# Kernel tuning notes

Measured on AMD Instinct MI355X. Metric: run time of the kernel, lower is better.

The kernel has to match this reference:

```python
import jax, jax.numpy as jnp
import numpy as np

N = 100000
E = 1600000
NODE_DIM = 64
H = 128
NUM_LAYERS = 3
NUM_CLASSES = 6
NUM_GRAPHS = 512
LN_EPS = 1e-5


def setup_inputs() -> dict:
    key = jax.random.key(0)
    ks = jax.random.split(key, 16)
    s = 0.05
    x = jax.random.normal(ks[0], (N, NODE_DIM), jnp.float32)
    edge_index = jax.random.randint(ks[1], (2, E), 0, N, dtype=jnp.int64)
    batch = jnp.sort(jax.random.randint(ks[2], (N,), 0, NUM_GRAPHS, dtype=jnp.int64))
    return {
        "x": x,
        "edge_index": edge_index,
        "batch": batch,
        "proj_w": jax.random.normal(ks[3], (NODE_DIM, H), jnp.float32) * s,
        "proj_b": jnp.zeros((H,), jnp.float32),
        "lin_l_w": jax.random.normal(ks[4], (NUM_LAYERS, H, H), jnp.float32) * s,
        "lin_l_b": jnp.zeros((NUM_LAYERS, H), jnp.float32),
        "lin_r_w": jax.random.normal(ks[5], (NUM_LAYERS, H, H), jnp.float32) * s,
        "ln_g": jnp.ones((NUM_LAYERS, H), jnp.float32),
        "ln_b": jnp.zeros((NUM_LAYERS, H), jnp.float32),
        "gate_w1": jax.random.normal(ks[6], (H, H // 2), jnp.float32) * s,
        "gate_b1": jnp.zeros((H // 2,), jnp.float32),
        "gate_w2": jax.random.normal(ks[7], (H // 2, 1), jnp.float32) * s,
        "gate_b2": jnp.zeros((1,), jnp.float32),
        "cls_w1": jax.random.normal(ks[8], (H, H // 2), jnp.float32) * s,
        "cls_b1": jnp.zeros((H // 2,), jnp.float32),
        "cls_w2": jax.random.normal(ks[9], (H // 2, NUM_CLASSES), jnp.float32) * s,
        "cls_b2": jnp.zeros((NUM_CLASSES,), jnp.float32),
    }


def _layer_norm(x, g, b):
    mu = jnp.mean(x, axis=-1, keepdims=True)
    var = jnp.mean(jnp.square(x - mu), axis=-1, keepdims=True)
    return (x - mu) * jax.lax.rsqrt(var + LN_EPS) * g + b


def _sage_mean_aggr(x, src, dst):
    # mean of source node features grouped by destination node
    summed = jax.ops.segment_sum(x[src], dst, num_segments=N)  # [N,H]
    deg = jax.ops.segment_sum(jnp.ones((E,), x.dtype), dst, num_segments=N)
    return summed / jnp.maximum(deg, 1.0)[:, None]


def reference(x, edge_index, batch, proj_w, proj_b, lin_l_w, lin_l_b, lin_r_w,
              ln_g, ln_b, gate_w1, gate_b1, gate_w2, gate_b2,
              cls_w1, cls_b1, cls_w2, cls_b2):
    src, dst = edge_index[0], edge_index[1]
    h = jax.nn.relu(x @ proj_w + proj_b)  # [N,H]
    for l in range(NUM_LAYERS):
        r = h
        aggr = _sage_mean_aggr(h, src, dst)
        # PyG SAGEConv: lin_l(aggregated) + lin_r(self), bias only in lin_l
        h = aggr @ lin_l_w[l] + lin_l_b[l] + h @ lin_r_w[l]
        h = _layer_norm(h, ln_g[l], ln_b[l])
        h = jax.nn.elu(h)
        h = h + r  # dropout is identity in eval mode
    # GlobalAttention pooling: segment softmax over nodes per graph
    gate = (jax.nn.relu(h @ gate_w1 + gate_b1) @ gate_w2 + gate_b2)[:, 0]  # [N]
    gmax = jax.ops.segment_max(gate, batch, num_segments=NUM_GRAPHS)
    eg = jnp.exp(gate - gmax[batch])
    denom = jax.ops.segment_sum(eg, batch, num_segments=NUM_GRAPHS)
    alpha = eg / denom[batch]  # [N]
    pooled = jax.ops.segment_sum(h * alpha[:, None], batch, num_segments=NUM_GRAPHS)  # [G,H]
    out = jax.nn.relu(pooled @ cls_w1 + cls_b1) @ cls_w2 + cls_b2  # [G,C]
    return out
```

## Files before the change

### kernel.cpp

```cpp
#include <hip/hip_runtime.h>
#include <hip/hip_fp16.h>
#include <math.h>

#define N_NODES   100000
#define N_EDGES   1600000
#define NDIM      64
#define H         128
#define NUM_LAYERS 3
#define NUM_CLASSES 6
#define NUM_GRAPHS 512
#define LN_EPS    1e-5f
#define NBKT      391
#define SCAP      5376
#define BPAD      136

typedef _Float16 f16x8 __attribute__((ext_vector_type(8)));
typedef float    f32x4 __attribute__((ext_vector_type(4)));

__device__ __forceinline__ int idx_at(const int* raw, int is64, int i) {
    return is64 ? raw[2 * (long long)i] : raw[i];
}
__device__ __forceinline__ int lower_bound(const int* a, int n, int v) {
    int lo = 0, hi = n;
    while (lo < hi) { int m = (lo + hi) >> 1; if (a[m] < v) lo = m + 1; else hi = m; }
    return lo;
}

__global__ void k_detect(const int* eraw, const int* braw, int* flags) {
    if (threadIdx.x == 0 && blockIdx.x == 0) {
        int e64 = 1;
        for (int i = 1; i < 128; i += 2) if (eraw[i] != 0) { e64 = 0; break; }
        flags[0] = e64;
        flags[1] = (braw[N_NODES - 1] == 0) ? 1 : 0;
    }
}

__global__ void k_init(int* bcnt) {
    int i = blockIdx.x * blockDim.x + threadIdx.x;
    if (i < 512) bcnt[i] = 0;
}

__global__ void k_conv_batch(const int* braw, const int* flags, int* batch32) {
    int i = blockIdx.x * blockDim.x + threadIdx.x;
    if (i < N_NODES) batch32[i] = idx_at(braw, flags[1], i);
}

__global__ __launch_bounds__(256) void k_bhist(const int* eraw, const int* flags, int* bcnt) {
    __shared__ int c[512];
    int tid = threadIdx.x;
    for (int i = tid; i < 512; i += 256) c[i] = 0;
    __syncthreads();
    int f = flags[0];
    int stride = gridDim.x * 256;
    for (int e = blockIdx.x * 256 + tid; e < N_EDGES; e += stride) {
        int d = idx_at(eraw, f, N_EDGES + e);
        atomicAdd(&c[d >> 8], 1);
    }
    __syncthreads();
    for (int i = tid; i < 512; i += 256) if (c[i]) atomicAdd(&bcnt[i], c[i]);
}

__global__ void k_bscan(const int* bcnt, int* boff, int* bcursor) {
    __shared__ int sh[512];
    int tid = threadIdx.x;
    int v = bcnt[tid];
    sh[tid] = v;
    __syncthreads();
    for (int off = 1; off < 512; off <<= 1) {
        int u = (tid >= off) ? sh[tid - off] : 0;
        __syncthreads();
        sh[tid] += u;
        __syncthreads();
    }
    int excl = sh[tid] - v;
    boff[tid] = excl;
    bcursor[tid] = excl;
    if (tid == 511) boff[512] = sh[511];
}

#define EPB 4096
__global__ __launch_bounds__(256) void k_bucket(const int* eraw, const int* flags,
                                                int* bcursor, unsigned int* br) {
    __shared__ int cnt[512];
    __shared__ int lcur[512];
    int tid = threadIdx.x;
    int f = flags[0];
    int base = blockIdx.x * EPB;
    int se[16], de[16];
#pragma unroll
    for (int j = 0; j < 16; ++j) {
        int e = base + j * 256 + tid;
        if (e < N_EDGES) {
            se[j] = idx_at(eraw, f, e);
            de[j] = idx_at(eraw, f, N_EDGES + e);
        } else de[j] = -1;
    }
    for (int i = tid; i < 512; i += 256) cnt[i] = 0;
    __syncthreads();
#pragma unroll
    for (int j = 0; j < 16; ++j)
        if (de[j] >= 0) atomicAdd(&cnt[de[j] >> 8], 1);
    __syncthreads();
    for (int i = tid; i < 512; i += 256)
        lcur[i] = cnt[i] ? atomicAdd(&bcursor[i], cnt[i]) : 0;
    __syncthreads();
#pragma unroll
    for (int j = 0; j < 16; ++j)
        if (de[j] >= 0) {
            int pos = atomicAdd(&lcur[de[j] >> 8], 1);
            br[pos] = ((unsigned int)(de[j] & 255) << 24) | (unsigned int)se[j];
        }
}

__global__ __launch_bounds__(256) void k_csr_tail(const unsigned int* br, const int* boff,
                                                  int* rowptr, int* col) {
    __shared__ int d256[256];
    __shared__ int sc[256];
    __shared__ int cbuf[SCAP];
    int b = blockIdx.x;
    int tid = threadIdx.x;
    int lo = boff[b], hi = boff[b + 1];
    int wsize = hi - lo;
    d256[tid] = 0;
    __syncthreads();
    for (int i = lo + tid; i < hi; i += 256)
        atomicAdd(&d256[br[i] >> 24], 1);
    __syncthreads();
    int v = d256[tid];
    sc[tid] = v;
    __syncthreads();
    for (int off = 1; off < 256; off <<= 1) {
        int u = (tid >= off) ? sc[tid - off] : 0;
        __syncthreads();
        sc[tid] += u;
        __syncthreads();
    }
    int excl = sc[tid] - v;
    int node = (b << 8) + tid;
    if (node < N_NODES) rowptr[node] = lo + excl;
    if (b == NBKT - 1 && tid == 0) rowptr[N_NODES] = N_EDGES;
    __syncthreads();
    d256[tid] = excl;
    __syncthreads();
    if (wsize <= SCAP) {
        for (int i = lo + tid; i < hi; i += 256) {
            unsigned int r = br[i];
            int p = atomicAdd(&d256[r >> 24], 1);
            cbuf[p] = (int)(r & 0xFFFFFF);
        }
        __syncthreads();
        for (int j = tid; j < wsize; j += 256) col[lo + j] = cbuf[j] << 8;
    } else {
        for (int i = lo + tid; i < hi; i += 256) {
            unsigned int r = br[i];
            int p = atomicAdd(&d256[r >> 24], 1);
            col[lo + p] = (int)(r & 0xFFFFFF) << 8;
        }
    }
}

__global__ void k_prepw(const float* __restrict__ lin_l_w, const float* __restrict__ lin_r_w,
                        const float* __restrict__ gate_w1,
                        __half* __restrict__ W16t, __half* __restrict__ W16g) {
    int i = blockIdx.x * 256 + threadIdx.x;
    if (i < NUM_LAYERS * 128 * 256) {
        int l = i >> 15;
        int rem = i & 32767;
        int n = rem >> 8;
        int k = rem & 255;
        float v = (k < 128) ? lin_l_w[(size_t)l * 16384 + k * 128 + n]
                            : lin_r_w[(size_t)l * 16384 + (k - 128) * 128 + n];
        W16t[(size_t)l * 32768 + n * 256 + k] = __float2half(v);
    } else if (i < NUM_LAYERS * 128 * 256 + 64 * 128) {
        int idx = i - NUM_LAYERS * 128 * 256;
        int n = idx >> 7;
        int k = idx & 127;
        W16g[n * 128 + k] = __float2half(gate_w1[k * 64 + n]);
    }
}

__global__ __launch_bounds__(256) void k_gemm_proj(const float* __restrict__ A,
                                                   const float* __restrict__ W,
                                                   const float* __restrict__ bias,
                                                   __half* __restrict__ C16,
                                                   int nrows, int K) {
    __shared__ float As_t[32][68];
    __shared__ float Ws[32 * 128];
    int tid = threadIdx.x;
    int row0 = blockIdx.x * 64;
    int tr = tid >> 4;
    int tc = tid & 15;
    int c0 = tc * 8;
    float acc[4][8];
#pragma unroll
    for (int i = 0; i < 4; ++i)
#pragma unroll
        for (int j = 0; j < 8; ++j) acc[i][j] = 0.f;

    for (int kc = 0; kc < K; kc += 32) {
        __syncthreads();
#pragma unroll
        for (int it = 0; it < 2; ++it) {
            int idx = tid + it * 256;
            int r = idx >> 3, c4 = idx & 7;
            int gr = row0 + r;
            float4 v = make_float4(0.f, 0.f, 0.f, 0.f);
            if (gr < nrows) v = *(const float4*)(A + (size_t)gr * K + kc + c4 * 4);
            As_t[c4 * 4 + 0][r] = v.x;
            As_t[c4 * 4 + 1][r] = v.y;
            As_t[c4 * 4 + 2][r] = v.z;
            As_t[c4 * 4 + 3][r] = v.w;
        }
#pragma unroll
        for (int it = 0; it < 4; ++it) {
            int idx = tid + it * 256;
            int r = idx >> 5, c4 = idx & 31;
            *(float4*)(&Ws[r * 128 + c4 * 4]) = *(const float4*)(W + (size_t)(kc + r) * 128 + c4 * 4);
        }
        __syncthreads();
#pragma unroll
        for (int k = 0; k < 32; ++k) {
            float4 a4 = *(const float4*)(&As_t[k][tr * 4]);
            float a[4] = {a4.x, a4.y, a4.z, a4.w};
            float4 w0 = *(const float4*)(&Ws[k * 128 + c0]);
            float4 w1 = *(const float4*)(&Ws[k * 128 + c0 + 4]);
            float w[8] = {w0.x, w0.y, w0.z, w0.w, w1.x, w1.y, w1.z, w1.w};
#pragma unroll
            for (int i = 0; i < 4; ++i)
#pragma unroll
                for (int j = 0; j < 8; ++j) acc[i][j] += a[i] * w[j];
        }
    }
    float bv[8];
#pragma unroll
    for (int j = 0; j < 8; ++j) bv[j] = bias[c0 + j];
#pragma unroll
    for (int i = 0; i < 4; ++i) {
        int gr = row0 + tr * 4 + i;
        if (gr < nrows) {
            float o[8];
#pragma unroll
            for (int j = 0; j < 8; ++j) o[j] = fmaxf(acc[i][j] + bv[j], 0.f);
            __half2 p[4];
#pragma unroll
            for (int j = 0; j < 8; j += 2) p[j / 2] = __floats2half2_rn(o[j], o[j + 1]);
            *(float4*)(C16 + (size_t)gr * 128 + c0) = *(float4*)p;
        }
    }
}

__global__ __launch_bounds__(256) void k_gate_mfma(const __half* __restrict__ h16,
                                                   const __half* __restrict__ W16g,
                                                   const float* __restrict__ b1,
                                                   const float* __restrict__ w2,
                                                   const float* __restrict__ b2,
                                                   float* __restrict__ gate) {
    __shared__ __half Bs[64 * BPAD];
    int tid = threadIdx.x;
    int wave = tid >> 6, lane = tid & 63;
    int s = lane & 15, quad = lane >> 4;
    int row0 = blockIdx.x * 64 + wave * 16;
    int arow = row0 + s;
    if (arow >= N_NODES) arow = N_NODES - 1;

#pragma unroll
    for (int it = 0; it < 4; ++it) {
        int idx = tid + it * 256;
        int n = idx >> 4, ch = idx & 15;
        *(float4*)(&Bs[n * BPAD + ch * 8]) = *(const float4*)(W16g + (size_t)n * 128 + ch * 8);
    }
    __syncthreads();

    f32x4 acc[4];
#pragma unroll
    for (int c = 0; c < 4; ++c) acc[c] = (f32x4){0.f, 0.f, 0.f, 0.f};

    const __half* aptr = h16 + (size_t)arow * H;
#pragma unroll
    for (int kc = 0; kc < 128; kc += 32) {
        f16x8 afrag = *(const f16x8*)(aptr + kc + quad * 8);
#pragma unroll
        for (int c = 0; c < 4; ++c) {
            f16x8 bfrag = *(const f16x8*)(&Bs[(c * 16 + s) * BPAD + kc + quad * 8]);
            acc[c] = __builtin_amdgcn_mfma_f32_16x16x32_f16(afrag, bfrag, acc[c], 0, 0, 0);
        }
    }
    float part[4] = {0.f, 0.f, 0.f, 0.f};
#pragma unroll
    for (int c = 0; c < 4; ++c) {
        float bv = b1[c * 16 + s];
        float wv = w2[c * 16 + s];
#pragma unroll
        for (int i = 0; i < 4; ++i)
            part[i] += fmaxf(acc[c][i] + bv, 0.f) * wv;
    }
#pragma unroll
    for (int off = 1; off < 16; off <<= 1) {
#pragma unroll
        for (int i = 0; i < 4; ++i) part[i] += __shfl_xor(part[i], off);
    }
    if (s == 0) {
        float b2v = b2[0];
#pragma unroll
        for (int i = 0; i < 4; ++i) {
            int r = row0 + quad * 4 + i;
            if (r < N_NODES) gate[r] = part[i] + b2v;
        }
    }
}

__global__ __launch_bounds__(64) void k_softmax_g(float* __restrict__ gate,
                                                  const int* __restrict__ batch32,
                                                  float* __restrict__ gsum) {
    int g = blockIdx.x;
    int lane = threadIdx.x;
    int n0 = lower_bound(batch32, N_NODES, g);
    int n1 = lower_bound(batch32, N_NODES, g + 1);
    float m = -INFINITY;
    for (int n = n0 + lane; n < n1; n += 64) m = fmaxf(m, gate[n]);
#pragma unroll
    for (int off = 32; off >= 1; off >>= 1) m = fmaxf(m, __shfl_xor(m, off));
    float s = 0.f;
    for (int n = n0 + lane; n < n1; n += 64) {
        float e = expf(gate[n] - m);
        gate[n] = e;
        s += e;
    }
#pragma unroll
    for (int off = 32; off >= 1; off >>= 1) s += __shfl_xor(s, off);
    if (lane == 0) gsum[g] = s;
}

__global__ __launch_bounds__(256) void k_pool_g(const __half* __restrict__ h16,
                                                const float* __restrict__ eg,
                                                const float* __restrict__ gsum,
                                                const int* __restrict__ batch32,
                                                float* __restrict__ pooled) {
    __shared__ float sacc[256];
    int g = blockIdx.x;
    int tid = threadIdx.x;
    int c = tid & 127;
    int p = tid >> 7;
    int n0 = lower_bound(batch32, N_NODES, g);
    int n1 = lower_bound(batch32, N_NODES, g + 1);
    float acc = 0.f;
    for (int n = n0 + p; n < n1; n += 2)
        acc += eg[n] * __half2float(h16[(size_t)n * H + c]);
    sacc[tid] = acc;
    __syncthreads();
    if (tid < 128) {
        float s = gsum[g];
        float v = sacc[tid] + sacc[tid + 128];
        pooled[(size_t)g * H + tid] = (n1 > n0) ? v / s : 0.f;
    }
}

__global__ __launch_bounds__(256) void k_layer_mfma(const __half* __restrict__ t16,
                                                    __half* __restrict__ h16,
                                                    const __half* __restrict__ W16t,
                                                    const float* __restrict__ bl,
                                                    const float* __restrict__ g,
                                                    const float* __restrict__ bb) {
    __shared__ __half Bs[128 * BPAD];
    int tid = threadIdx.x;
    int wave = tid >> 6, lane = tid & 63;
    int s = lane & 15, quad = lane >> 4;
    int row0 = blockIdx.x * 64;
    int wrow0 = row0 + wave * 16;
    int arow = wrow0 + s;
    if (arow >= N_NODES) arow = N_NODES - 1;

    f32x4 acc[8];
#pragma unroll
    for (int c = 0; c < 8; ++c) acc[c] = (f32x4){0.f, 0.f, 0.f, 0.f};

#pragma unroll
    for (int ph = 0; ph < 2; ++ph) {
        __syncthreads();
#pragma unroll
        for (int it = 0; it < 8; ++it) {
            int idx = tid + it * 256;
            int n = idx >> 4, ch = idx & 15;
            *(float4*)(&Bs[n * BPAD + ch * 8]) =
                *(const float4*)(W16t + (size_t)n * 256 + ph * 128 + ch * 8);
        }
        __syncthreads();
        const __half* aptr = (ph ? h16 : t16) + (size_t)arow * H;
#pragma unroll
        for (int kk = 0; kk < 128; kk += 32) {
            f16x8 afrag = *(const f16x8*)(aptr + kk + quad * 8);
#pragma unroll
            for (int c = 0; c < 8; ++c) {
                f16x8 bfrag = *(const f16x8*)(&Bs[(c * 16 + s) * BPAD + kk + quad * 8]);
                acc[c] = __builtin_amdgcn_mfma_f32_16x16x32_f16(afrag, bfrag, acc[c], 0, 0, 0);
            }
        }
    }

    float y[8][4];
    float sm[4] = {0.f, 0.f, 0.f, 0.f}, sq[4] = {0.f, 0.f, 0.f, 0.f};
#pragma unroll
    for (int c = 0; c < 8; ++c) {
        float bv = bl[c * 16 + s];
#pragma unroll
        for (int i = 0; i < 4; ++i) {
            float v = acc[c][i] + bv;
            y[c][i] = v;
            sm[i] += v;
            sq[i] += v * v;
        }
    }
#pragma unroll
    for (int off = 1; off < 16; off <<= 1) {
#pragma unroll
        for (int i = 0; i < 4; ++i) {
            sm[i] += __shfl_xor(sm[i], off);
            sq[i] += __shfl_xor(sq[i], off);
        }
    }
    float mean[4], rstd[4];
#pragma unroll
    for (int i = 0; i < 4; ++i) {
        mean[i] = sm[i] * (1.0f / H);
        float var = sq[i] * (1.0f / H) - mean[i] * mean[i];
        rstd[i] = rsqrtf(var + LN_EPS);
    }
    float gv[8], bbv[8];
#pragma unroll
    for (int c = 0; c < 8; ++c) { gv[c] = g[c * 16 + s]; bbv[c] = bb[c * 16 + s]; }

    __syncthreads();
#pragma unroll
    for (int i = 0; i < 4; ++i) {
        int lr = wave * 16 + quad * 4 + i;
#pragma unroll
        for (int c = 0; c < 8; ++c) {
            float yv = (y[c][i] - mean[i]) * rstd[i] * gv[c] + bbv[c];
            yv = yv > 0.f ? yv : expf(yv) - 1.f;
            Bs[lr * BPAD + c * 16 + s] = __float2half(yv);
        }
    }
    __syncthreads();
#pragma unroll
    for (int it = 0; it < 4; ++it) {
        int idx = tid + it * 256;
        int r = idx >> 4, ch = idx & 15;
        int grow = row0 + r;
        if (grow < N_NODES) {
            float4 sv = *(float4*)(&Bs[r * BPAD + ch * 8]);
            float4 hv = *(const float4*)(h16 + (size_t)grow * H + ch * 8);
            __half2* pa = (__half2*)&sv;
            const __half2* pb = (const __half2*)&hv;
#pragma unroll
            for (int j = 0; j < 4; ++j) {
                float2 fa = __half22float2(pa[j]);
                float2 fb = __half22float2(pb[j]);
                pa[j] = __floats2half2_rn(fa.x + fb.x, fa.y + fb.y);
            }
            *(float4*)(h16 + (size_t)grow * H + ch * 8) = sv;
        }
    }
}

__global__ __launch_bounds__(256) void k_aggr(const __half* __restrict__ h16,
                                              const int* __restrict__ rowptr,
                                              const int* __restrict__ col,
                                              __half* __restrict__ t16) {
    int lane = threadIdx.x & 63;
    int node = blockIdx.x * 4 + (threadIdx.x >> 6);
    if (node >= N_NODES) return;
    int s = lane & 15;
    int g = lane >> 4;
    int e0 = rowptr[node];
    int deg = rowptr[node + 1] - e0;
    const char* hb = (const char*)h16 + s * 16;

    __half2 z = __floats2half2_rn(0.f, 0.f);
    __half2 ac[4][4];
#pragma unroll
    for (int a = 0; a < 4; ++a)
#pragma unroll
        for (int k = 0; k < 4; ++k) ac[a][k] = z;

    for (int base = 0; base < deg; base += 64) {
        int rem = deg - base;
        int cvv = (lane < rem) ? col[e0 + base + lane] : 0;
#pragma unroll
        for (int half = 0; half < 2; ++half) {
            int h32 = half * 32;
            if (h32 >= rem) break;
            float4 rv[8];
            bool act[8];
#pragma unroll
            for (int j = 0; j < 8; ++j) {
                int ei = h32 + g + 4 * j;
                act[j] = ei < rem;
                int cb = __shfl(cvv, ei);
                if (act[j]) rv[j] = *(const float4*)(hb + cb);
            }
#pragma unroll
            for (int j = 0; j < 8; ++j) {
                if (act[j]) {
                    const __half2* hv = (const __half2*)&rv[j];
                    int a = j & 3;
                    ac[a][0] = __hadd2(ac[a][0], hv[0]);
                    ac[a][1] = __hadd2(ac[a][1], hv[1]);
                    ac[a][2] = __hadd2(ac[a][2], hv[2]);
                    ac[a][3] = __hadd2(ac[a][3], hv[3]);
                }
            }
        }
    }

    float f[8];
#pragma unroll
    for (int k = 0; k < 4; ++k) {
        float2 s0 = __half22float2(ac[0][k]);
        float2 s1 = __half22float2(ac[1][k]);
        float2 s2 = __half22float2(ac[2][k]);
        float2 s3 = __half22float2(ac[3][k]);
        f[2 * k]     = (s0.x + s1.x) + (s2.x + s3.x);
        f[2 * k + 1] = (s0.y + s1.y) + (s2.y + s3.y);
    }
#pragma unroll
    for (int off = 16; off <= 32; off <<= 1) {
#pragma unroll
        for (int k = 0; k < 8; ++k) f[k] += __shfl_xor(f[k], off);
    }
    if (g == 0) {
        float inv = 1.0f / (float)(deg > 1 ? deg : 1);
        __half2 o[4];
#pragma unroll
        for (int k = 0; k < 4; ++k)
            o[k] = __floats2half2_rn(f[2 * k] * inv, f[2 * k + 1] * inv);
        *(float4*)(t16 + (size_t)node * H + s * 8) = *(float4*)o;
    }
}

__global__ __launch_bounds__(64) void k_cls(const float* __restrict__ pooled,
                                            const float* __restrict__ w1,
                                            const float* __restrict__ b1,
                                            const float* __restrict__ w2,
                                            const float* __restrict__ b2,
                                            float* __restrict__ out) {
    __shared__ float sp[64];
    int g = blockIdx.x;
    int lane = threadIdx.x;
    float r0 = pooled[(size_t)g * H + lane];
    float r1 = pooled[(size_t)g * H + 64 + lane];
    float acc = b1[lane];
#pragma unroll 16
    for (int k = 0; k < 64; ++k) acc += __shfl(r0, k) * w1[k * 64 + lane];
#pragma unroll 16
    for (int k = 0; k < 64; ++k) acc += __shfl(r1, k) * w1[(64 + k) * 64 + lane];
    sp[lane] = fmaxf(acc, 0.f);
    __syncthreads();
    if (lane < NUM_CLASSES) {
        float o = b2[lane];
        for (int c = 0; c < 64; ++c) o += sp[c] * w2[c * NUM_CLASSES + lane];
        out[g * NUM_CLASSES + lane] = o;
    }
}

extern "C" void kernel_launch(void* const* d_in, const int* in_sizes, int n_in,
                              void* d_out, int out_size, void* d_ws, size_t ws_size,
                              hipStream_t stream) {
    const float* x       = (const float*)d_in[0];
    const int*   eraw    = (const int*)d_in[1];
    const int*   braw    = (const int*)d_in[2];
    const float* proj_w  = (const float*)d_in[3];
    const float* proj_b  = (const float*)d_in[4];
    const float* lin_l_w = (const float*)d_in[5];
    const float* lin_l_b = (const float*)d_in[6];
    const float* lin_r_w = (const float*)d_in[7];
    const float* ln_g    = (const float*)d_in[8];
    const float* ln_b    = (const float*)d_in[9];
    const float* gate_w1 = (const float*)d_in[10];
    const float* gate_b1 = (const float*)d_in[11];
    const float* gate_w2 = (const float*)d_in[12];
    const float* gate_b2 = (const float*)d_in[13];
    const float* cls_w1  = (const float*)d_in[14];
    const float* cls_b1  = (const float*)d_in[15];
    const float* cls_w2  = (const float*)d_in[16];
    const float* cls_b2  = (const float*)d_in[17];
    float* out = (float*)d_out;

    __half* h16    = (__half*)d_ws;
    __half* t16    = h16 + (size_t)N_NODES * H;
    float*  gate   = (float*)(t16 + (size_t)N_NODES * H);
    float*  gsum   = gate + N_NODES;
    float*  pooled = gsum + NUM_GRAPHS;
    __half* W16t   = (__half*)(pooled + NUM_GRAPHS * H);
    __half* W16g   = W16t + (size_t)NUM_LAYERS * 32768;
    int* flags     = (int*)(W16g + 64 * 128);
    int* col       = flags + 4;
    int* batch32   = col + N_EDGES;
    int* rowptr    = batch32 + N_NODES;
    int* bcnt      = rowptr + N_NODES + 1;
    int* boff      = bcnt + 512;
    int* bcursor   = boff + 513;
    unsigned int* br = (unsigned int*)(bcursor + 512);

    const int nbN = (N_NODES + 255) / 256;
    const int nbE4 = (N_EDGES + EPB - 1) / EPB;
    const int nbW = (N_NODES + 3) / 4;
    const int nbG = (N_NODES + 63) / 64;
    const int nbP = (NUM_LAYERS * 128 * 256 + 64 * 128 + 255) / 256;

    k_detect<<<1, 1, 0, stream>>>(eraw, braw, flags);
    k_init<<<2, 256, 0, stream>>>(bcnt);
    k_conv_batch<<<nbN, 256, 0, stream>>>(braw, flags, batch32);
    k_bhist<<<512, 256, 0, stream>>>(eraw, flags, bcnt);
    k_bscan<<<1, 512, 0, stream>>>(bcnt, boff, bcursor);
    k_bucket<<<nbE4, 256, 0, stream>>>(eraw, flags, bcursor, br);
    k_csr_tail<<<NBKT, 256, 0, stream>>>(br, boff, rowptr, col);
    k_prepw<<<nbP, 256, 0, stream>>>(lin_l_w, lin_r_w, gate_w1, W16t, W16g);

    k_gemm_proj<<<nbG, 256, 0, stream>>>(x, proj_w, proj_b, h16, N_NODES, NDIM);

    for (int l = 0; l < NUM_LAYERS; ++l) {
        const float* bl  = lin_l_b + (size_t)l * H;
        const float* gl  = ln_g + (size_t)l * H;
        const float* blb = ln_b + (size_t)l * H;
        k_aggr<<<nbW, 256, 0, stream>>>(h16, rowptr, col, t16);
        k_layer_mfma<<<nbG, 256, 0, stream>>>(t16, h16, W16t + (size_t)l * 32768, bl, gl, blb);
    }

    k_gate_mfma<<<nbG, 256, 0, stream>>>(h16, W16g, gate_b1, gate_w2, gate_b2, gate);
    k_softmax_g<<<NUM_GRAPHS, 64, 0, stream>>>(gate, batch32, gsum);
    k_pool_g<<<NUM_GRAPHS, 256, 0, stream>>>(h16, gate, gsum, batch32, pooled);
    k_cls<<<NUM_GRAPHS, 64, 0, stream>>>(pooled, cls_w1, cls_b1, cls_w2, cls_b2, out);
}
```

Baseline: 489.7 us.

## Make neighbor aggregation persistent with prefetch and branchless zero-row gathers

The aggregation kernel now runs on a fixed grid of 1280 blocks. Each wave walks nodes with a grid stride, loading the rowptr and column indices of the next two nodes while it gathers the current node. Out-of-range edge slots now point at a zeroed 256-byte region, reusing the start of the gate buffer cleared in k_init, so gathers run unpredicated instead of being masked per edge. This aims to hide index-load latency and remove branch and predication overhead. In exchange it reads some wasted zero rows for low-degree nodes, uses more registers under the new occupancy hint, and relies on the gate buffer staying zero until the gate kernel runs.

```diff
diff --git a/kernel.cpp b/kernel.cpp
--- a/kernel.cpp
+++ b/kernel.cpp
@@ -13,6 +13,7 @@
 #define NBKT      391
 #define SCAP      5376
 #define BPAD      136
+#define NBLK_AGGR 1280
 
 typedef _Float16 f16x8 __attribute__((ext_vector_type(8)));
 typedef float    f32x4 __attribute__((ext_vector_type(4)));
@@ -35,9 +36,10 @@
     }
 }
 
-__global__ void k_init(int* bcnt) {
+__global__ void k_init(int* bcnt, float* gate_z) {
     int i = blockIdx.x * blockDim.x + threadIdx.x;
     if (i < 512) bcnt[i] = 0;
+    if (i < 64) gate_z[i] = 0.f;
 }
 
 __global__ void k_conv_batch(const int* braw, const int* flags, int* batch32) {
@@ -462,45 +464,73 @@
     }
 }
 
-__global__ __launch_bounds__(256) void k_aggr(const __half* __restrict__ h16,
-                                              const int* __restrict__ rowptr,
-                                              const int* __restrict__ col,
-                                              __half* __restrict__ t16) {
+__global__ __launch_bounds__(256, 5) void k_aggr(const __half* __restrict__ h16,
+                                                 const int* __restrict__ rowptr,
+                                                 const int* __restrict__ col,
+                                                 __half* __restrict__ t16,
+                                                 int zoff) {
     int lane = threadIdx.x & 63;
-    int node = blockIdx.x * 4 + (threadIdx.x >> 6);
-    if (node >= N_NODES) return;
+    int wid = blockIdx.x * 4 + (threadIdx.x >> 6);
+    const int NW = NBLK_AGGR * 4;
     int s = lane & 15;
     int g = lane >> 4;
+    const char* hb = (const char*)h16 + s * 16;
+
+    int node = wid;
+    if (node >= N_NODES) return;
+
     int e0 = rowptr[node];
     int deg = rowptr[node + 1] - e0;
-    const char* hb = (const char*)h16 + s * 16;
-
-    __half2 z = __floats2half2_rn(0.f, 0.f);
-    __half2 ac[4][4];
-#pragma unroll
-    for (int a = 0; a < 4; ++a)
-#pragma unroll
-        for (int k = 0; k < 4; ++k) ac[a][k] = z;
-
-    for (int base = 0; base < deg; base += 64) {
-        int rem = deg - base;
-        int cvv = (lane < rem) ? col[e0 + base + lane] : 0;
-#pragma unroll
-        for (int half = 0; half < 2; ++half) {
-            int h32 = half * 32;
-            if (h32 >= rem) break;
+    int cv = (lane < deg) ? col[e0 + lane] : zoff;
+    int n1 = node + NW;
+    int f0 = 0, ndeg = 0;
+    if (n1 < N_NODES) { f0 = rowptr[n1]; ndeg = rowptr[n1 + 1] - f0; }
+
+    while (true) {
+        int n2 = n1 + NW;
+        int p0 = 0, pdeg = 0;
+        if (n2 < N_NODES) { p0 = rowptr[n2]; pdeg = rowptr[n2 + 1] - p0; }
+        int ncv = zoff;
+        if (n1 < N_NODES && lane < ndeg) ncv = col[f0 + lane];
+
+        __half2 z = __floats2half2_rn(0.f, 0.f);
+        __half2 ac[4][4];
+#pragma unroll
+        for (int a = 0; a < 4; ++a)
+#pragma unroll
+            for (int k = 0; k < 4; ++k) ac[a][k] = z;
+
+        int r64 = deg < 64 ? deg : 64;
+        for (int h32 = 0; h32 < r64; h32 += 32) {
             float4 rv[8];
-            bool act[8];
 #pragma unroll
             for (int j = 0; j < 8; ++j) {
-                int ei = h32 + g + 4 * j;
-                act[j] = ei < rem;
-                int cb = __shfl(cvv, ei);
-                if (act[j]) rv[j] = *(const float4*)(hb + cb);
+                int cb = __shfl(cv, h32 + g + 4 * j);
+                rv[j] = *(const float4*)(hb + cb);
             }
 #pragma unroll
             for (int j = 0; j < 8; ++j) {
-                if (act[j]) {
+                const __half2* hv = (const __half2*)&rv[j];
+                int a = j & 3;
+                ac[a][0] = __hadd2(ac[a][0], hv[0]);
+                ac[a][1] = __hadd2(ac[a][1], hv[1]);
+                ac[a][2] = __hadd2(ac[a][2], hv[2]);
+                ac[a][3] = __hadd2(ac[a][3], hv[3]);
+            }
+        }
+        for (int base = 64; base < deg; base += 64) {
+            int rem = deg - base;
+            int cvv = (lane < rem) ? col[e0 + base + lane] : zoff;
+            int rr = rem < 64 ? rem : 64;
+            for (int h32 = 0; h32 < rr; h32 += 32) {
+                float4 rv[8];
+#pragma unroll
+                for (int j = 0; j < 8; ++j) {
+                    int cb = __shfl(cvv, h32 + g + 4 * j);
+                    rv[j] = *(const float4*)(hb + cb);
+                }
+#pragma unroll
+                for (int j = 0; j < 8; ++j) {
                     const __half2* hv = (const __half2*)&rv[j];
                     int a = j & 3;
                     ac[a][0] = __hadd2(ac[a][0], hv[0]);
@@ -510,30 +540,34 @@
                 }
             }
         }
-    }
-
-    float f[8];
-#pragma unroll
-    for (int k = 0; k < 4; ++k) {
-        float2 s0 = __half22float2(ac[0][k]);
-        float2 s1 = __half22float2(ac[1][k]);
-        float2 s2 = __half22float2(ac[2][k]);
-        float2 s3 = __half22float2(ac[3][k]);
-        f[2 * k]     = (s0.x + s1.x) + (s2.x + s3.x);
-        f[2 * k + 1] = (s0.y + s1.y) + (s2.y + s3.y);
-    }
-#pragma unroll
-    for (int off = 16; off <= 32; off <<= 1) {
-#pragma unroll
-        for (int k = 0; k < 8; ++k) f[k] += __shfl_xor(f[k], off);
-    }
-    if (g == 0) {
-        float inv = 1.0f / (float)(deg > 1 ? deg : 1);
-        __half2 o[4];
-#pragma unroll
-        for (int k = 0; k < 4; ++k)
-            o[k] = __floats2half2_rn(f[2 * k] * inv, f[2 * k + 1] * inv);
-        *(float4*)(t16 + (size_t)node * H + s * 8) = *(float4*)o;
+
+        float f[8];
+#pragma unroll
+        for (int k = 0; k < 4; ++k) {
+            float2 s0 = __half22float2(ac[0][k]);
+            float2 s1 = __half22float2(ac[1][k]);
+            float2 s2 = __half22float2(ac[2][k]);
+            float2 s3 = __half22float2(ac[3][k]);
+            f[2 * k]     = (s0.x + s1.x) + (s2.x + s3.x);
+            f[2 * k + 1] = (s0.y + s1.y) + (s2.y + s3.y);
+        }
+#pragma unroll
+        for (int off = 16; off <= 32; off <<= 1) {
+#pragma unroll
+            for (int k = 0; k < 8; ++k) f[k] += __shfl_xor(f[k], off);
+        }
+        if (g == 0) {
+            float inv = 1.0f / (float)(deg > 1 ? deg : 1);
+            __half2 o[4];
+#pragma unroll
+            for (int k = 0; k < 4; ++k)
+                o[k] = __floats2half2_rn(f[2 * k] * inv, f[2 * k + 1] * inv);
+            *(float4*)(t16 + (size_t)node * H + s * 8) = *(float4*)o;
+        }
+
+        if (n1 >= N_NODES) break;
+        node = n1; deg = ndeg; cv = ncv; e0 = f0;
+        n1 = n2; f0 = p0; ndeg = pdeg;
     }
 }
 
@@ -601,14 +635,15 @@
     int* bcursor   = boff + 513;
     unsigned int* br = (unsigned int*)(bcursor + 512);
 
+    const int zoff = (int)((const char*)gate - (const char*)h16);
+
     const int nbN = (N_NODES + 255) / 256;
     const int nbE4 = (N_EDGES + EPB - 1) / EPB;
-    const int nbW = (N_NODES + 3) / 4;
     const int nbG = (N_NODES + 63) / 64;
     const int nbP = (NUM_LAYERS * 128 * 256 + 64 * 128 + 255) / 256;
 
     k_detect<<<1, 1, 0, stream>>>(eraw, braw, flags);
-    k_init<<<2, 256, 0, stream>>>(bcnt);
+    k_init<<<2, 256, 0, stream>>>(bcnt, gate);
     k_conv_batch<<<nbN, 256, 0, stream>>>(braw, flags, batch32);
     k_bhist<<<512, 256, 0, stream>>>(eraw, flags, bcnt);
     k_bscan<<<1, 512, 0, stream>>>(bcnt, boff, bcursor);
@@ -622,7 +657,7 @@
         const float* bl  = lin_l_b + (size_t)l * H;
         const float* gl  = ln_g + (size_t)l * H;
         const float* blb = ln_b + (size_t)l * H;
-        k_aggr<<<nbW, 256, 0, stream>>>(h16, rowptr, col, t16);
+        k_aggr<<<NBLK_AGGR, 256, 0, stream>>>(h16, rowptr, col, t16, zoff);
         k_layer_mfma<<<nbG, 256, 0, stream>>>(t16, h16, W16t + (size_t)l * 32768, bl, gl, blb);
     }
 
```

Result: slower. 501.8 us (+2.5%).
